# Kernel tuning notes

Hardware: AMD Instinct MI355X
Metric: run time of the kernel (lower is better)

## Reference

```python
import jax, jax.numpy as jnp
import numpy as np
from jax import lax

# dims from init_kwargs: in_features=1920, out_features=1920, window_size=12
B = 1024
IN_F = 1920
OUT_F = 1920
WS = 12              # window_size (GRU input & hidden size)
K = IN_F // WS
OUT_WS = OUT_F // K  # per-block decoder output = 12
D_HID = 1024         # decoder hidden width


def sinusoidal_pe(L, d):
    # standard sinusoidal positional encoding, shape (L, d)
    pos = jnp.arange(L, dtype=jnp.float32)[:, None]
    div = jnp.exp(jnp.arange(0, d, 2, dtype=jnp.float32) * (-np.log(10000.0) / d))
    ang = pos * div  # (L, d//2)
    pe = jnp.zeros((L, d), jnp.float32)
    pe = pe.at[:, 0::2].set(jnp.sin(ang))
    pe = pe.at[:, 1::2].set(jnp.cos(ang))
    return pe


def gru(x, h0, Wih, Whh, bih, bhh):
    # x: (B, T, I) batch_first; PyTorch GRU gate order: r, z, n
    def step(h, xt):
        gi = xt @ Wih.T + bih          # (B, 3H)
        gh = h @ Whh.T + bhh           # (B, 3H)
        ir, iz, inn = jnp.split(gi, 3, axis=-1)
        hr, hz, hn = jnp.split(gh, 3, axis=-1)
        r = jax.nn.sigmoid(ir + hr)
        z = jax.nn.sigmoid(iz + hz)
        n = jnp.tanh(inn + r * hn)
        h_new = (1.0 - z) * n + z * h
        return h_new, h_new
    hT, ys = lax.scan(step, h0, jnp.swapaxes(x, 0, 1))
    return jnp.swapaxes(ys, 0, 1), hT


def setup_inputs() -> dict:
    key = jax.random.key(0)
    ks = jax.random.split(key, 11)
    s = lambda k, shape: jax.random.normal(k, shape, jnp.float32) * 0.05
    return {
        "x": jax.random.normal(ks[0], (B, IN_F), jnp.float32),
        # per-block segment encoders: Linear(WS, WS) x K
        "enc_W": s(ks[1], (K, WS, WS)),
        "enc_b": s(ks[2], (K, WS)),
        # shared GRU (input=hidden=WS)
        "Wih": s(ks[3], (3 * WS, WS)),
        "Whh": s(ks[4], (3 * WS, WS)),
        "bih": s(ks[5], (3 * WS,)),
        "bhh": s(ks[6], (3 * WS,)),
        # per-block decoders: Linear(WS,1024) -> Linear(1024,OUT_WS)
        "dec_W1": s(ks[7], (K, WS, D_HID)),
        "dec_b1": s(ks[8], (K, D_HID)),
        "dec_W2": s(ks[9], (K, D_HID, OUT_WS)),
        "dec_b2": s(ks[10], (K, OUT_WS)),
    }


def reference(x, enc_W, enc_b, Wih, Whh, bih, bhh, dec_W1, dec_b1, dec_W2, dec_b2):
    # SegmentationBlock: split (B, IN_F) -> (B, K, WS), per-block Linear+ReLU
    xb = x.reshape(B, K, WS)
    xs = jax.nn.relu(jnp.einsum('bki,kio->bko', xb, enc_W) + enc_b[None])

    # first GRU pass: only final hidden state h (B, WS)
    h0 = jnp.zeros((B, WS), x.dtype)
    _, h = gru(xs, h0, Wih, Whh, bih, bhh)

    # positional encodings (value-independent sinusoidal, broadcast over batch)
    pos_enc = sinusoidal_pe(K, WS)          # (K, WS)
    ch_pe = sinusoidal_pe(K, K)             # (K, K)
    # channel_enc[:, :, j] = channel_encs[:, :, j // K]  (fused gather)
    channel_enc = ch_pe[:, jnp.arange(WS) // K]  # (K, WS)

    x_enc = xs + pos_enc[None] + channel_enc[None]

    # second GRU pass initialized with h
    out, _ = gru(x_enc, h, Wih, Whh, bih, bhh)  # (B, K, WS)

    # per-block decoder MLPs (dropout is identity in eval)
    hid = jnp.einsum('bkd,kdh->bkh', out, dec_W1) + dec_b1[None]      # (B, K, 1024)
    res = jnp.einsum('bkh,kho->bko', hid, dec_W2) + dec_b2[None]      # (B, K, OUT_WS)
    return res.reshape(B, K * OUT_WS)[:, :OUT_F]
```

## Files before the change

kernel.cpp:

```cpp
#include <hip/hip_runtime.h>
#include <hip/hip_bf16.h>

using bf16 = __hip_bfloat16;
typedef float v2f __attribute__((ext_vector_type(2)));

#define C1 1.44269504f
#define C2 2.88539008f

__device__ __forceinline__ float fexp2(float x) { return __builtin_amdgcn_exp2f(x); }
__device__ __forceinline__ float frcp(float x)  { return __builtin_amdgcn_rcpf(x); }

__device__ __forceinline__ unsigned int f2bfbits(float f) {
    union { float f; unsigned int u; } c; c.f = f;
    return (c.u + 0x7fffu + ((c.u >> 16) & 1u)) >> 16;
}

#define KSTR 12288
#define OFF_PEGI 15728640

__global__ __launch_bounds__(256) void k_encode(
    const float* __restrict__ x, const float* __restrict__ encW, const float* __restrict__ encb,
    const float* __restrict__ Wih, const float* __restrict__ bih, const float* __restrict__ bhh,
    uint2* __restrict__ gi, float4* __restrict__ pegi)
{
    const int k = blockIdx.y, t = threadIdx.x;
    const int b = blockIdx.x * 256 + t;

    __shared__ float sW[144], sbm[12], sWih[432], sbih[36], spet[12];
    __shared__ uint2 st[256 * 13];
    if (t < 144) sW[t]  = encW[k * 144 + t];
    if (t < 12)  sbm[t] = encb[k * 12 + t];
    for (int i = t; i < 432; i += 256) sWih[i] = Wih[i];
    if (t < 36)  sbih[t] = bih[t] + (t < 24 ? bhh[t] : 0.f);
    if (t < 12) {
        int m = t >> 1;
        float div = __expf((float)(2 * m) * (-0.7675283643313489f));
        float ang = (float)k * div;
        spet[t] = ((t & 1) ? cosf(ang) : sinf(ang)) + sinf((float)k);
    }
    __syncthreads();
    if (t < 12 && blockIdx.x == 0) {
        float sr = 0.f, sz = 0.f, sn = 0.f;
        #pragma unroll
        for (int o = 0; o < 12; o++) {
            sr = fmaf(spet[o], sWih[t * 12 + o], sr);
            sz = fmaf(spet[o], sWih[(12 + t) * 12 + o], sz);
            sn = fmaf(spet[o], sWih[(24 + t) * 12 + o], sn);
        }
        pegi[k * 12 + t] = make_float4(C1 * sr, C1 * sz, C2 * sn, 0.f);
    }

    const float4* xp = reinterpret_cast<const float4*>(x + (size_t)b * 1920 + k * 12);
    float4 a0 = xp[0], a1 = xp[1], a2 = xp[2];
    float xv[12] = {a0.x,a0.y,a0.z,a0.w, a1.x,a1.y,a1.z,a1.w, a2.x,a2.y,a2.z,a2.w};

    float xs[12];
    #pragma unroll
    for (int o = 0; o < 12; o++) {
        float s = sbm[o];
        #pragma unroll
        for (int i = 0; i < 12; i++) s = fmaf(xv[i], sW[i * 12 + o], s);
        xs[o] = fmaxf(s, 0.f);
    }

    #pragma unroll
    for (int j = 0; j < 12; j++) {
        float sr = sbih[j], sz = sbih[12 + j], sn = sbih[24 + j];
        #pragma unroll
        for (int o = 0; o < 12; o++) {
            sr = fmaf(xs[o], sWih[j * 12 + o], sr);
            sz = fmaf(xs[o], sWih[(12 + j) * 12 + o], sz);
            sn = fmaf(xs[o], sWih[(24 + j) * 12 + o], sn);
        }
        st[t * 13 + j] = make_uint2(f2bfbits(C1 * sr) | (f2bfbits(C1 * sz) << 16),
                                    f2bfbits(C2 * sn));
    }
    __syncthreads();
    uint2* gbase = gi + (size_t)k * KSTR + (size_t)blockIdx.x * 3072;
    for (int i = t; i < 3072; i += 256) {
        int bl = i / 12;
        gbase[i] = st[bl * 13 + (i - bl * 12)];
    }
}

__global__ __launch_bounds__(64) void k_recur(
    const float* __restrict__ Whh, const float* __restrict__ bhh,
    const uint2* __restrict__ gi, const float4* __restrict__ pegi,
    float* __restrict__ hout)
{
    const int lane = threadIdx.x;
    const int ju = (lane < 12) ? lane : 11;
    const int b = blockIdx.x;

    v2f wr2[6], wz2[6], wn2[6];
    #pragma unroll
    for (int i = 0; i < 6; i++) {
        wr2[i] = (v2f){C1 * Whh[ju * 12 + 2*i],        C1 * Whh[ju * 12 + 2*i + 1]};
        wz2[i] = (v2f){C1 * Whh[(12 + ju) * 12 + 2*i], C1 * Whh[(12 + ju) * 12 + 2*i + 1]};
        wn2[i] = (v2f){C2 * Whh[(24 + ju) * 12 + 2*i], C2 * Whh[(24 + ju) * 12 + 2*i + 1]};
    }
    const float bn = C2 * bhh[24 + ju];

    const uint2* gp = gi + (size_t)b * 12 + ju;

    v2f hs2[6];
    #pragma unroll
    for (int i = 0; i < 6; i++) hs2[i] = (v2f){0.f, 0.f};
    float hself = 0.f, p = 1.f;

    uint2 buf[8];
    #pragma unroll
    for (int i = 0; i < 8; i++) buf[i] = gp[(size_t)i * KSTR];

    for (int ko = 0; ko < 160; ko += 8) {
        #pragma unroll
        for (int i = 0; i < 8; i++) {
            const int k = ko + i;
            const int kp = (k + 8 > 159) ? 159 : k + 8;
            float gr = __int_as_float((int)(buf[i].x << 16));
            float gz = __int_as_float((int)(buf[i].x & 0xffff0000u));
            float gn = __int_as_float((int)(buf[i].y << 16));
            buf[i] = gp[(size_t)kp * KSTR];
            v2f an = (v2f){bn, 0.f};
            v2f ar = (v2f){gr, 0.f};
            v2f az = (v2f){gz, 0.f};
            #pragma unroll
            for (int d = 0; d < 6; d++) an += wn2[d] * hs2[d];
            #pragma unroll
            for (int d = 0; d < 6; d++) { ar += wr2[d] * hs2[d]; az += wz2[d] * hs2[d]; }
            float hr = ar.x + ar.y;
            float hz = az.x + az.y;
            float hn = an.x + an.y;
            float r = frcp(1.f + fexp2(-hr));
            float w = frcp(1.f + fexp2(hz));
            float t = fmaf(r, hn, gn);
            float e = frcp(1.f + fexp2(t));
            float hj = fmaf(w, fmaf(-2.f, e, p), hself);
            hself = hj; p = 1.f - hj;
            int hv = __float_as_int(hj);
            #pragma unroll
            for (int d = 0; d < 6; d++)
                hs2[d] = (v2f){__int_as_float(__builtin_amdgcn_readlane(hv, 2*d)),
                               __int_as_float(__builtin_amdgcn_readlane(hv, 2*d + 1))};
        }
    }

    const float4* pp = pegi + ju;
    float4 pb[8];
    #pragma unroll
    for (int i = 0; i < 8; i++) {
        buf[i] = gp[(size_t)i * KSTR];
        pb[i]  = pp[i * 12];
    }
    float* ho = hout + (size_t)b * 1920;
    for (int ko = 0; ko < 160; ko += 8) {
        #pragma unroll
        for (int i = 0; i < 8; i++) {
            const int k = ko + i;
            const int kp = (k + 8 > 159) ? 159 : k + 8;
            float gr = __int_as_float((int)(buf[i].x << 16))         + pb[i].x;
            float gz = __int_as_float((int)(buf[i].x & 0xffff0000u)) + pb[i].y;
            float gn = __int_as_float((int)(buf[i].y << 16))         + pb[i].z;
            buf[i] = gp[(size_t)kp * KSTR];
            pb[i]  = pp[kp * 12];
            v2f an = (v2f){bn, 0.f};
            v2f ar = (v2f){gr, 0.f};
            v2f az = (v2f){gz, 0.f};
            #pragma unroll
            for (int d = 0; d < 6; d++) an += wn2[d] * hs2[d];
            #pragma unroll
            for (int d = 0; d < 6; d++) { ar += wr2[d] * hs2[d]; az += wz2[d] * hs2[d]; }
            float hr = ar.x + ar.y;
            float hz = az.x + az.y;
            float hn = an.x + an.y;
            float r = frcp(1.f + fexp2(-hr));
            float w = frcp(1.f + fexp2(hz));
            float t = fmaf(r, hn, gn);
            float e = frcp(1.f + fexp2(t));
            float hj = fmaf(w, fmaf(-2.f, e, p), hself);
            hself = hj; p = 1.f - hj;
            if (lane < 12) ho[k * 12 + lane] = hj;
            int hv = __float_as_int(hj);
            #pragma unroll
            for (int d = 0; d < 6; d++)
                hs2[d] = (v2f){__int_as_float(__builtin_amdgcn_readlane(hv, 2*d)),
                               __int_as_float(__builtin_amdgcn_readlane(hv, 2*d + 1))};
        }
    }
}

__global__ __launch_bounds__(256) void k_foldapply(
    const float* __restrict__ W1, const float* __restrict__ b1,
    const float* __restrict__ W2, const float* __restrict__ b2,
    float* __restrict__ out)
{
    const int k = blockIdx.x, t = threadIdx.x;
    __shared__ float sB[12288];
    __shared__ float sb1[1024];
    __shared__ float sWc[144], sbc[12];
    {
        const float4* w2p = reinterpret_cast<const float4*>(W2 + (size_t)k * 12288);
        float4* sB4 = reinterpret_cast<float4*>(sB);
        for (int i = t; i < 3072; i += 256) sB4[i] = w2p[i];
        const float4* b1p = reinterpret_cast<const float4*>(b1 + (size_t)k * 1024);
        float4* sb14 = reinterpret_cast<float4*>(sb1);
        sb14[t] = b1p[t];
    }
    __syncthreads();
    if (t < 156) {
        const int o = (t < 144) ? (t % 12) : (t - 144);
        float s0 = 0.f, s1 = 0.f, s2 = 0.f, s3 = 0.f;
        if (t < 144) {
            const float4* va4 = reinterpret_cast<const float4*>(W1 + (size_t)k * 12288 + (size_t)(t / 12) * 1024);
            #pragma unroll 4
            for (int q = 0; q < 256; q++) {
                float4 a = va4[q];
                const float* bq = sB + q * 48 + o;
                s0 = fmaf(a.x, bq[0],  s0);
                s1 = fmaf(a.y, bq[12], s1);
                s2 = fmaf(a.z, bq[24], s2);
                s3 = fmaf(a.w, bq[36], s3);
            }
        } else {
            #pragma unroll 4
            for (int hh = 0; hh < 1024; hh += 4) {
                const float* bq = sB + hh * 12 + o;
                s0 = fmaf(sb1[hh],     bq[0],  s0);
                s1 = fmaf(sb1[hh + 1], bq[12], s1);
                s2 = fmaf(sb1[hh + 2], bq[24], s2);
                s3 = fmaf(sb1[hh + 3], bq[36], s3);
            }
        }
        float s = (s0 + s1) + (s2 + s3);
        if (t < 144) sWc[t] = s;
        else         sbc[t - 144] = s + b2[k * 12 + o];
    }
    __syncthreads();

    for (int bb = t; bb < 1024; bb += 256) {
        float* hp = out + (size_t)bb * 1920 + k * 12;
        float4* h4 = reinterpret_cast<float4*>(hp);
        float4 a0 = h4[0], a1 = h4[1], a2 = h4[2];
        float hv[12] = {a0.x,a0.y,a0.z,a0.w, a1.x,a1.y,a1.z,a1.w, a2.x,a2.y,a2.z,a2.w};
        float ov[12];
        #pragma unroll
        for (int o = 0; o < 12; o++) {
            float s = sbc[o];
            #pragma unroll
            for (int d = 0; d < 12; d++) s = fmaf(hv[d], sWc[d * 12 + o], s);
            ov[o] = s;
        }
        h4[0] = make_float4(ov[0], ov[1], ov[2],  ov[3]);
        h4[1] = make_float4(ov[4], ov[5], ov[6],  ov[7]);
        h4[2] = make_float4(ov[8], ov[9], ov[10], ov[11]);
    }
}

extern "C" void kernel_launch(void* const* d_in, const int* in_sizes, int n_in,
                              void* d_out, int out_size, void* d_ws, size_t ws_size,
                              hipStream_t stream)
{
    const float* x    = (const float*)d_in[0];
    const float* encW = (const float*)d_in[1];
    const float* encb = (const float*)d_in[2];
    const float* Wih  = (const float*)d_in[3];
    const float* Whh  = (const float*)d_in[4];
    const float* bih  = (const float*)d_in[5];
    const float* bhh  = (const float*)d_in[6];
    const float* W1   = (const float*)d_in[7];
    const float* b1   = (const float*)d_in[8];
    const float* W2   = (const float*)d_in[9];
    const float* b2   = (const float*)d_in[10];
    float* out = (float*)d_out;

    char* ws = (char*)d_ws;
    uint2*  gi   = (uint2*)(ws);
    float4* pegi = (float4*)(ws + OFF_PEGI);

    k_encode   <<<dim3(4, 160), 256, 0, stream>>>(x, encW, encb, Wih, bih, bhh, gi, pegi);
    k_recur    <<<dim3(1024),   64,  0, stream>>>(Whh, bhh, gi, pegi, out);
    k_foldapply<<<dim3(160),    256, 0, stream>>>(W1, b1, W2, b2, out);
}
```

Baseline: 188.3 us.

## Pack four batch rows per wavefront in GRU recurrence using ds_bpermute broadcast

The recurrence kernel now handles four batch samples per 64-lane wavefront, one per 16-lane group, instead of one sample using only 12 of 64 lanes. Each lane gets the hidden state of its own group through ds_bpermute, which replaces the scalar readlane broadcast, and the grid shrinks from 1024 to 256 blocks. This fills more of each wave and cuts the number of waves, but it puts an LDS-crossbar permute with its latency on the serial per-step dependency chain.

```diff
diff --git a/kernel.cpp b/kernel.cpp
--- a/kernel.cpp
+++ b/kernel.cpp
@@ -89,8 +89,14 @@
     float* __restrict__ hout)
 {
     const int lane = threadIdx.x;
-    const int ju = (lane < 12) ? lane : 11;
-    const int b = blockIdx.x;
+    const int grp  = lane >> 4;
+    const int j    = lane & 15;
+    const int ju   = (j < 12) ? j : 11;
+    const int b    = blockIdx.x * 4 + grp;
+
+    int ba[12];
+    #pragma unroll
+    for (int d = 0; d < 12; d++) ba[d] = ((lane & 48) + d) << 2;
 
     v2f wr2[6], wz2[6], wn2[6];
     #pragma unroll
@@ -101,16 +107,16 @@
     }
     const float bn = C2 * bhh[24 + ju];
 
-    const uint2* gp = gi + (size_t)b * 12 + ju;
-
-    v2f hs2[6];
-    #pragma unroll
-    for (int i = 0; i < 6; i++) hs2[i] = (v2f){0.f, 0.f};
+    const int voff = b * 12 + ju;
+
+    v2f h2[6];
+    #pragma unroll
+    for (int i = 0; i < 6; i++) h2[i] = (v2f){0.f, 0.f};
     float hself = 0.f, p = 1.f;
 
     uint2 buf[8];
     #pragma unroll
-    for (int i = 0; i < 8; i++) buf[i] = gp[(size_t)i * KSTR];
+    for (int i = 0; i < 8; i++) buf[i] = gi[(size_t)i * KSTR + voff];
 
     for (int ko = 0; ko < 160; ko += 8) {
         #pragma unroll
@@ -120,14 +126,14 @@
             float gr = __int_as_float((int)(buf[i].x << 16));
             float gz = __int_as_float((int)(buf[i].x & 0xffff0000u));
             float gn = __int_as_float((int)(buf[i].y << 16));
-            buf[i] = gp[(size_t)kp * KSTR];
+            buf[i] = gi[(size_t)kp * KSTR + voff];
             v2f an = (v2f){bn, 0.f};
             v2f ar = (v2f){gr, 0.f};
             v2f az = (v2f){gz, 0.f};
             #pragma unroll
-            for (int d = 0; d < 6; d++) an += wn2[d] * hs2[d];
-            #pragma unroll
-            for (int d = 0; d < 6; d++) { ar += wr2[d] * hs2[d]; az += wz2[d] * hs2[d]; }
+            for (int d = 0; d < 6; d++) an += wn2[d] * h2[d];
+            #pragma unroll
+            for (int d = 0; d < 6; d++) { ar += wr2[d] * h2[d]; az += wz2[d] * h2[d]; }
             float hr = ar.x + ar.y;
             float hz = az.x + az.y;
             float hn = an.x + an.y;
@@ -140,19 +146,18 @@
             int hv = __float_as_int(hj);
             #pragma unroll
             for (int d = 0; d < 6; d++)
-                hs2[d] = (v2f){__int_as_float(__builtin_amdgcn_readlane(hv, 2*d)),
-                               __int_as_float(__builtin_amdgcn_readlane(hv, 2*d + 1))};
-        }
-    }
-
-    const float4* pp = pegi + ju;
+                h2[d] = (v2f){__int_as_float(__builtin_amdgcn_ds_bpermute(ba[2*d],     hv)),
+                              __int_as_float(__builtin_amdgcn_ds_bpermute(ba[2*d + 1], hv))};
+        }
+    }
+
     float4 pb[8];
     #pragma unroll
     for (int i = 0; i < 8; i++) {
-        buf[i] = gp[(size_t)i * KSTR];
-        pb[i]  = pp[i * 12];
-    }
-    float* ho = hout + (size_t)b * 1920;
+        buf[i] = gi[(size_t)i * KSTR + voff];
+        pb[i]  = pegi[i * 12 + ju];
+    }
+    const int hoff = b * 1920 + j;
     for (int ko = 0; ko < 160; ko += 8) {
         #pragma unroll
         for (int i = 0; i < 8; i++) {
@@ -161,15 +166,15 @@
             float gr = __int_as_float((int)(buf[i].x << 16))         + pb[i].x;
             float gz = __int_as_float((int)(buf[i].x & 0xffff0000u)) + pb[i].y;
             float gn = __int_as_float((int)(buf[i].y << 16))         + pb[i].z;
-            buf[i] = gp[(size_t)kp * KSTR];
-            pb[i]  = pp[kp * 12];
+            buf[i] = gi[(size_t)kp * KSTR + voff];
+            pb[i]  = pegi[kp * 12 + ju];
             v2f an = (v2f){bn, 0.f};
             v2f ar = (v2f){gr, 0.f};
             v2f az = (v2f){gz, 0.f};
             #pragma unroll
-            for (int d = 0; d < 6; d++) an += wn2[d] * hs2[d];
-            #pragma unroll
-            for (int d = 0; d < 6; d++) { ar += wr2[d] * hs2[d]; az += wz2[d] * hs2[d]; }
+            for (int d = 0; d < 6; d++) an += wn2[d] * h2[d];
+            #pragma unroll
+            for (int d = 0; d < 6; d++) { ar += wr2[d] * h2[d]; az += wz2[d] * h2[d]; }
             float hr = ar.x + ar.y;
             float hz = az.x + az.y;
             float hn = an.x + an.y;
@@ -179,12 +184,12 @@
             float e = frcp(1.f + fexp2(t));
             float hj = fmaf(w, fmaf(-2.f, e, p), hself);
             hself = hj; p = 1.f - hj;
-            if (lane < 12) ho[k * 12 + lane] = hj;
+            if (j < 12) hout[hoff + k * 12] = hj;
             int hv = __float_as_int(hj);
             #pragma unroll
             for (int d = 0; d < 6; d++)
-                hs2[d] = (v2f){__int_as_float(__builtin_amdgcn_readlane(hv, 2*d)),
-                               __int_as_float(__builtin_amdgcn_readlane(hv, 2*d + 1))};
+                h2[d] = (v2f){__int_as_float(__builtin_amdgcn_ds_bpermute(ba[2*d],     hv)),
+                              __int_as_float(__builtin_amdgcn_ds_bpermute(ba[2*d + 1], hv))};
         }
     }
 }
@@ -278,6 +283,6 @@
     float4* pegi = (float4*)(ws + OFF_PEGI);
 
     k_encode   <<<dim3(4, 160), 256, 0, stream>>>(x, encW, encb, Wih, bih, bhh, gi, pegi);
-    k_recur    <<<dim3(1024),   64,  0, stream>>>(Whh, bhh, gi, pegi, out);
+    k_recur    <<<dim3(256),    64,  0, stream>>>(Whh, bhh, gi, pegi, out);
     k_foldapply<<<dim3(160),    256, 0, stream>>>(W1, b1, W2, b2, out);
 }
```

New measurement: 198.0 us. +5.1%, slower.

## Run GRU recurrence on MFMA with 16 batch rows per wave and fused decoder

Applied to the files above, without the earlier changes.

The GRU hidden-state matvec is rewritten as fp16 16x16x16 MFMA ops, so each 64-lane wave advances 16 batch rows at once instead of one row per wave with readlane broadcasts. The encoder now writes gate inputs in an MFMA-friendly bf16 layout, and the folded decoder weights are packed to fp16 and applied inside the recurrence, which removes the separate read-modify-write pass over the output. The grid shrinks from 1024 waves to 64, which cuts total work but leaves far fewer waves to hide the serial step latency. fp16 weights and hidden state lower precision.

```diff
diff --git a/kernel.cpp b/kernel.cpp
--- a/kernel.cpp
+++ b/kernel.cpp
@@ -2,32 +2,40 @@
 #include <hip/hip_bf16.h>
 
 using bf16 = __hip_bfloat16;
-typedef float v2f __attribute__((ext_vector_type(2)));
+typedef __fp16 half2_t __attribute__((ext_vector_type(2)));
+typedef __fp16 half4_t __attribute__((ext_vector_type(4)));
+typedef float  f4_t    __attribute__((ext_vector_type(4)));
 
 #define C1 1.44269504f
 #define C2 2.88539008f
 
 __device__ __forceinline__ float fexp2(float x) { return __builtin_amdgcn_exp2f(x); }
 __device__ __forceinline__ float frcp(float x)  { return __builtin_amdgcn_rcpf(x); }
-
 __device__ __forceinline__ unsigned int f2bfbits(float f) {
     union { float f; unsigned int u; } c; c.f = f;
     return (c.u + 0x7fffu + ((c.u >> 16) & 1u)) >> 16;
 }
-
-#define KSTR 12288
-#define OFF_PEGI 15728640
+__device__ __forceinline__ unsigned int pk2(float a, float b) {
+    return f2bfbits(a) | (f2bfbits(b) << 16);
+}
+__device__ __forceinline__ float blo(unsigned int u) { return __int_as_float((int)(u << 16)); }
+__device__ __forceinline__ float bhi(unsigned int u) { return __int_as_float((int)(u & 0xffff0000u)); }
+
+#define OFF_GIN  10485760
+#define OFF_PERZ 15728640
+#define OFF_PEN  15892480
+#define OFF_WCA  15974400
 
 __global__ __launch_bounds__(256) void k_encode(
     const float* __restrict__ x, const float* __restrict__ encW, const float* __restrict__ encb,
     const float* __restrict__ Wih, const float* __restrict__ bih, const float* __restrict__ bhh,
-    uint2* __restrict__ gi, float4* __restrict__ pegi)
+    uint4* __restrict__ giRZ, uint2* __restrict__ giN,
+    uint4* __restrict__ peRZ, uint2* __restrict__ peN)
 {
     const int k = blockIdx.y, t = threadIdx.x;
     const int b = blockIdx.x * 256 + t;
 
-    __shared__ float sW[144], sbm[12], sWih[432], sbih[36], spet[12];
-    __shared__ uint2 st[256 * 13];
+    __shared__ float sW[144], sbm[12], sWih[432], sbih[36], spet[12], spe3[36];
     if (t < 144) sW[t]  = encW[k * 144 + t];
     if (t < 12)  sbm[t] = encb[k * 12 + t];
     for (int i = t; i < 432; i += 256) sWih[i] = Wih[i];
@@ -39,7 +47,7 @@
         spet[t] = ((t & 1) ? cosf(ang) : sinf(ang)) + sinf((float)k);
     }
     __syncthreads();
-    if (t < 12 && blockIdx.x == 0) {
+    if (t < 12) {
         float sr = 0.f, sz = 0.f, sn = 0.f;
         #pragma unroll
         for (int o = 0; o < 12; o++) {
@@ -47,7 +55,7 @@
             sz = fmaf(spet[o], sWih[(12 + t) * 12 + o], sz);
             sn = fmaf(spet[o], sWih[(24 + t) * 12 + o], sn);
         }
-        pegi[k * 12 + t] = make_float4(C1 * sr, C1 * sz, C2 * sn, 0.f);
+        spe3[t] = C1 * sr; spe3[12 + t] = C1 * sz; spe3[24 + t] = C2 * sn;
     }
 
     const float4* xp = reinterpret_cast<const float4*>(x + (size_t)b * 1920 + k * 12);
@@ -63,6 +71,7 @@
         xs[o] = fmaxf(s, 0.f);
     }
 
+    float r12[12], z12[12], n12[12];
     #pragma unroll
     for (int j = 0; j < 12; j++) {
         float sr = sbih[j], sz = sbih[12 + j], sn = sbih[24 + j];
@@ -72,127 +81,178 @@
             sz = fmaf(xs[o], sWih[(12 + j) * 12 + o], sz);
             sn = fmaf(xs[o], sWih[(24 + j) * 12 + o], sn);
         }
-        st[t * 13 + j] = make_uint2(f2bfbits(C1 * sr) | (f2bfbits(C1 * sz) << 16),
-                                    f2bfbits(C2 * sn));
+        r12[j] = C1 * sr; z12[j] = C1 * sz; n12[j] = C2 * sn;
     }
     __syncthreads();
-    uint2* gbase = gi + (size_t)k * KSTR + (size_t)blockIdx.x * 3072;
-    for (int i = t; i < 3072; i += 256) {
-        int bl = i / 12;
-        gbase[i] = st[bl * 13 + (i - bl * 12)];
+
+    if (blockIdx.x == 0 && t < 64) {
+        const int q = t >> 4;
+        float vr[4], vz[4], vn[4];
+        #pragma unroll
+        for (int i = 0; i < 4; i++) {
+            int row = 4 * q + i;
+            vr[i] = (row < 12) ? spe3[row]      : 0.f;
+            vz[i] = (row < 12) ? spe3[12 + row] : 0.f;
+            vn[i] = (row < 12) ? spe3[24 + row] : 0.f;
+        }
+        peRZ[k * 64 + t] = make_uint4(pk2(vr[0],vr[1]), pk2(vr[2],vr[3]),
+                                      pk2(vz[0],vz[1]), pk2(vz[2],vz[3]));
+        peN [k * 64 + t] = make_uint2(pk2(vn[0],vn[1]), pk2(vn[2],vn[3]));
+    }
+
+    const int c = b & 15, w = b >> 4;
+    const int base = (k * 64 + w) * 64 + c;
+    #pragma unroll
+    for (int g = 0; g < 3; g++) {
+        giRZ[base + 16 * g] = make_uint4(pk2(r12[4*g], r12[4*g+1]), pk2(r12[4*g+2], r12[4*g+3]),
+                                         pk2(z12[4*g], z12[4*g+1]), pk2(z12[4*g+2], z12[4*g+3]));
+        giN [base + 16 * g] = make_uint2(pk2(n12[4*g], n12[4*g+1]), pk2(n12[4*g+2], n12[4*g+3]));
     }
 }
 
 __global__ __launch_bounds__(64) void k_recur(
     const float* __restrict__ Whh, const float* __restrict__ bhh,
-    const uint2* __restrict__ gi, const float4* __restrict__ pegi,
-    float* __restrict__ hout)
+    const uint4* __restrict__ giRZ, const uint2* __restrict__ giN,
+    const uint4* __restrict__ peRZ, const uint2* __restrict__ peN,
+    const uint2* __restrict__ Wca, float* __restrict__ out)
 {
     const int lane = threadIdx.x;
-    const int ju = (lane < 12) ? lane : 11;
-    const int b = blockIdx.x;
-
-    v2f wr2[6], wz2[6], wn2[6];
-    #pragma unroll
-    for (int i = 0; i < 6; i++) {
-        wr2[i] = (v2f){C1 * Whh[ju * 12 + 2*i],        C1 * Whh[ju * 12 + 2*i + 1]};
-        wz2[i] = (v2f){C1 * Whh[(12 + ju) * 12 + 2*i], C1 * Whh[(12 + ju) * 12 + 2*i + 1]};
-        wn2[i] = (v2f){C2 * Whh[(24 + ju) * 12 + 2*i], C2 * Whh[(24 + ju) * 12 + 2*i + 1]};
-    }
-    const float bn = C2 * bhh[24 + ju];
-
-    const uint2* gp = gi + (size_t)b * 12 + ju;
-
-    v2f hs2[6];
-    #pragma unroll
-    for (int i = 0; i < 6; i++) hs2[i] = (v2f){0.f, 0.f};
-    float hself = 0.f, p = 1.f;
-
-    uint2 buf[8];
-    #pragma unroll
-    for (int i = 0; i < 8; i++) buf[i] = gp[(size_t)i * KSTR];
-
-    for (int ko = 0; ko < 160; ko += 8) {
-        #pragma unroll
-        for (int i = 0; i < 8; i++) {
+    const int c = lane & 15, q = lane >> 4;
+    const int wv = blockIdx.x;
+
+    union HU { half4_t h; half2_t p[2]; uint2 u; };
+    half4_t Ar, Az, An;
+    {
+        float vr[4], vz[4], vn[4];
+        #pragma unroll
+        for (int i = 0; i < 4; i++) {
+            int kd = 4 * q + i;
+            float fr = 0.f, fz = 0.f, fn = 0.f;
+            if (c < 12) {
+                if (kd < 12) {
+                    fr = C1 * Whh[c * 12 + kd];
+                    fz = C1 * Whh[(12 + c) * 12 + kd];
+                    fn = C2 * Whh[(24 + c) * 12 + kd];
+                } else if (kd == 12) {
+                    fn = C2 * bhh[24 + c];
+                }
+            }
+            vr[i] = fr; vz[i] = fz; vn[i] = fn;
+        }
+        HU ur, uz, un;
+        ur.p[0] = __builtin_amdgcn_cvt_pkrtz(vr[0], vr[1]);
+        ur.p[1] = __builtin_amdgcn_cvt_pkrtz(vr[2], vr[3]);
+        uz.p[0] = __builtin_amdgcn_cvt_pkrtz(vz[0], vz[1]);
+        uz.p[1] = __builtin_amdgcn_cvt_pkrtz(vz[2], vz[3]);
+        un.p[0] = __builtin_amdgcn_cvt_pkrtz(vn[0], vn[1]);
+        un.p[1] = __builtin_amdgcn_cvt_pkrtz(vn[2], vn[3]);
+        Ar = ur.h; Az = uz.h; An = un.h;
+    }
+
+    HU B;
+    B.u.x = (q < 3) ? 0u : 0x3C00u;
+    B.u.y = 0u;
+
+    float hsf[4] = {0.f, 0.f, 0.f, 0.f};
+    float pp [4] = {1.f, 1.f, 1.f, 1.f};
+    const f4_t zero4 = {0.f, 0.f, 0.f, 0.f};
+
+    uint4 gRZ[4]; uint2 gN[4];
+    #pragma unroll
+    for (int i = 0; i < 4; i++) {
+        gRZ[i] = giRZ[(i * 64 + wv) * 64 + lane];
+        gN [i] = giN [(i * 64 + wv) * 64 + lane];
+    }
+
+    for (int ko = 0; ko < 160; ko += 4) {
+        #pragma unroll
+        for (int i = 0; i < 4; i++) {
             const int k = ko + i;
-            const int kp = (k + 8 > 159) ? 159 : k + 8;
-            float gr = __int_as_float((int)(buf[i].x << 16));
-            float gz = __int_as_float((int)(buf[i].x & 0xffff0000u));
-            float gn = __int_as_float((int)(buf[i].y << 16));
-            buf[i] = gp[(size_t)kp * KSTR];
-            v2f an = (v2f){bn, 0.f};
-            v2f ar = (v2f){gr, 0.f};
-            v2f az = (v2f){gz, 0.f};
+            const int kp = (k + 4 > 159) ? 159 : k + 4;
+            f4_t Cr = {blo(gRZ[i].x), bhi(gRZ[i].x), blo(gRZ[i].y), bhi(gRZ[i].y)};
+            f4_t Cz = {blo(gRZ[i].z), bhi(gRZ[i].z), blo(gRZ[i].w), bhi(gRZ[i].w)};
+            float Gn[4] = {blo(gN[i].x), bhi(gN[i].x), blo(gN[i].y), bhi(gN[i].y)};
+            gRZ[i] = giRZ[(kp * 64 + wv) * 64 + lane];
+            gN [i] = giN [(kp * 64 + wv) * 64 + lane];
+            f4_t Dr = __builtin_amdgcn_mfma_f32_16x16x16f16(Ar, B.h, Cr, 0, 0, 0);
+            f4_t Dz = __builtin_amdgcn_mfma_f32_16x16x16f16(Az, B.h, Cz, 0, 0, 0);
+            f4_t Dn = __builtin_amdgcn_mfma_f32_16x16x16f16(An, B.h, zero4, 0, 0, 0);
             #pragma unroll
-            for (int d = 0; d < 6; d++) an += wn2[d] * hs2[d];
+            for (int ii = 0; ii < 4; ii++) {
+                float r  = frcp(1.f + fexp2(-Dr[ii]));
+                float w  = frcp(1.f + fexp2(Dz[ii]));
+                float tt = fmaf(r, Dn[ii], Gn[ii]);
+                float e  = frcp(1.f + fexp2(tt));
+                float s  = fmaf(-2.f, e, pp[ii]);
+                float hj = fmaf(w, s, hsf[ii]);
+                hsf[ii] = hj; pp[ii] = 1.f - hj;
+            }
+            HU nb;
+            nb.p[0] = __builtin_amdgcn_cvt_pkrtz(hsf[0], hsf[1]);
+            nb.p[1] = __builtin_amdgcn_cvt_pkrtz(hsf[2], hsf[3]);
+            B.u.x = (q < 3) ? nb.u.x : 0x3C00u;
+            B.u.y = (q < 3) ? nb.u.y : 0u;
+        }
+    }
+
+    uint4 pRZ[4]; uint2 pN[4]; uint2 wc[4];
+    #pragma unroll
+    for (int i = 0; i < 4; i++) {
+        gRZ[i] = giRZ[(i * 64 + wv) * 64 + lane];
+        gN [i] = giN [(i * 64 + wv) * 64 + lane];
+        pRZ[i] = peRZ[i * 64 + lane];
+        pN [i] = peN [i * 64 + lane];
+        wc [i] = Wca [i * 64 + lane];
+    }
+    float* orow = out + ((size_t)wv * 16 + c) * 1920 + 4 * q;
+    for (int ko = 0; ko < 160; ko += 4) {
+        #pragma unroll
+        for (int i = 0; i < 4; i++) {
+            const int k = ko + i;
+            const int kp = (k + 4 > 159) ? 159 : k + 4;
+            f4_t Cr = {blo(gRZ[i].x) + blo(pRZ[i].x), bhi(gRZ[i].x) + bhi(pRZ[i].x),
+                       blo(gRZ[i].y) + blo(pRZ[i].y), bhi(gRZ[i].y) + bhi(pRZ[i].y)};
+            f4_t Cz = {blo(gRZ[i].z) + blo(pRZ[i].z), bhi(gRZ[i].z) + bhi(pRZ[i].z),
+                       blo(gRZ[i].w) + blo(pRZ[i].w), bhi(gRZ[i].w) + bhi(pRZ[i].w)};
+            float Gn[4] = {blo(gN[i].x) + blo(pN[i].x), bhi(gN[i].x) + bhi(pN[i].x),
+                           blo(gN[i].y) + blo(pN[i].y), bhi(gN[i].y) + bhi(pN[i].y)};
+            HU adec; adec.u = wc[i];
+            gRZ[i] = giRZ[(kp * 64 + wv) * 64 + lane];
+            gN [i] = giN [(kp * 64 + wv) * 64 + lane];
+            pRZ[i] = peRZ[kp * 64 + lane];
+            pN [i] = peN [kp * 64 + lane];
+            wc [i] = Wca [kp * 64 + lane];
+            f4_t Dr = __builtin_amdgcn_mfma_f32_16x16x16f16(Ar, B.h, Cr, 0, 0, 0);
+            f4_t Dz = __builtin_amdgcn_mfma_f32_16x16x16f16(Az, B.h, Cz, 0, 0, 0);
+            f4_t Dn = __builtin_amdgcn_mfma_f32_16x16x16f16(An, B.h, zero4, 0, 0, 0);
             #pragma unroll
-            for (int d = 0; d < 6; d++) { ar += wr2[d] * hs2[d]; az += wz2[d] * hs2[d]; }
-            float hr = ar.x + ar.y;
-            float hz = az.x + az.y;
-            float hn = an.x + an.y;
-            float r = frcp(1.f + fexp2(-hr));
-            float w = frcp(1.f + fexp2(hz));
-            float t = fmaf(r, hn, gn);
-            float e = frcp(1.f + fexp2(t));
-            float hj = fmaf(w, fmaf(-2.f, e, p), hself);
-            hself = hj; p = 1.f - hj;
-            int hv = __float_as_int(hj);
-            #pragma unroll
-            for (int d = 0; d < 6; d++)
-                hs2[d] = (v2f){__int_as_float(__builtin_amdgcn_readlane(hv, 2*d)),
-                               __int_as_float(__builtin_amdgcn_readlane(hv, 2*d + 1))};
-        }
-    }
-
-    const float4* pp = pegi + ju;
-    float4 pb[8];
-    #pragma unroll
-    for (int i = 0; i < 8; i++) {
-        buf[i] = gp[(size_t)i * KSTR];
-        pb[i]  = pp[i * 12];
-    }
-    float* ho = hout + (size_t)b * 1920;
-    for (int ko = 0; ko < 160; ko += 8) {
-        #pragma unroll
-        for (int i = 0; i < 8; i++) {
-            const int k = ko + i;
-            const int kp = (k + 8 > 159) ? 159 : k + 8;
-            float gr = __int_as_float((int)(buf[i].x << 16))         + pb[i].x;
-            float gz = __int_as_float((int)(buf[i].x & 0xffff0000u)) + pb[i].y;
-            float gn = __int_as_float((int)(buf[i].y << 16))         + pb[i].z;
-            buf[i] = gp[(size_t)kp * KSTR];
-            pb[i]  = pp[kp * 12];
-            v2f an = (v2f){bn, 0.f};
-            v2f ar = (v2f){gr, 0.f};
-            v2f az = (v2f){gz, 0.f};
-            #pragma unroll
-            for (int d = 0; d < 6; d++) an += wn2[d] * hs2[d];
-            #pragma unroll
-            for (int d = 0; d < 6; d++) { ar += wr2[d] * hs2[d]; az += wz2[d] * hs2[d]; }
-            float hr = ar.x + ar.y;
-            float hz = az.x + az.y;
-            float hn = an.x + an.y;
-            float r = frcp(1.f + fexp2(-hr));
-            float w = frcp(1.f + fexp2(hz));
-            float t = fmaf(r, hn, gn);
-            float e = frcp(1.f + fexp2(t));
-            float hj = fmaf(w, fmaf(-2.f, e, p), hself);
-            hself = hj; p = 1.f - hj;
-            if (lane < 12) ho[k * 12 + lane] = hj;
-            int hv = __float_as_int(hj);
-            #pragma unroll
-            for (int d = 0; d < 6; d++)
-                hs2[d] = (v2f){__int_as_float(__builtin_amdgcn_readlane(hv, 2*d)),
-                               __int_as_float(__builtin_amdgcn_readlane(hv, 2*d + 1))};
-        }
-    }
-}
-
-__global__ __launch_bounds__(256) void k_foldapply(
+            for (int ii = 0; ii < 4; ii++) {
+                float r  = frcp(1.f + fexp2(-Dr[ii]));
+                float w  = frcp(1.f + fexp2(Dz[ii]));
+                float tt = fmaf(r, Dn[ii], Gn[ii]);
+                float e  = frcp(1.f + fexp2(tt));
+                float s  = fmaf(-2.f, e, pp[ii]);
+                float hj = fmaf(w, s, hsf[ii]);
+                hsf[ii] = hj; pp[ii] = 1.f - hj;
+            }
+            HU nb;
+            nb.p[0] = __builtin_amdgcn_cvt_pkrtz(hsf[0], hsf[1]);
+            nb.p[1] = __builtin_amdgcn_cvt_pkrtz(hsf[2], hsf[3]);
+            B.u.x = (q < 3) ? nb.u.x : 0x3C00u;
+            B.u.y = (q < 3) ? nb.u.y : 0u;
+            f4_t O = __builtin_amdgcn_mfma_f32_16x16x16f16(adec.h, B.h, zero4, 0, 0, 0);
+            if (q < 3) {
+                float4* op = reinterpret_cast<float4*>(orow + k * 12);
+                *op = make_float4(O[0], O[1], O[2], O[3]);
+            }
+        }
+    }
+}
+
+__global__ __launch_bounds__(256) void k_fold(
     const float* __restrict__ W1, const float* __restrict__ b1,
     const float* __restrict__ W2, const float* __restrict__ b2,
-    float* __restrict__ out)
+    uint2* __restrict__ Wca)
 {
     const int k = blockIdx.x, t = threadIdx.x;
     __shared__ float sB[12288];
@@ -213,9 +273,9 @@
         if (t < 144) {
             const float4* va4 = reinterpret_cast<const float4*>(W1 + (size_t)k * 12288 + (size_t)(t / 12) * 1024);
             #pragma unroll 4
-            for (int q = 0; q < 256; q++) {
-                float4 a = va4[q];
-                const float* bq = sB + q * 48 + o;
+            for (int qq = 0; qq < 256; qq++) {
+                float4 a = va4[qq];
+                const float* bq = sB + qq * 48 + o;
                 s0 = fmaf(a.x, bq[0],  s0);
                 s1 = fmaf(a.y, bq[12], s1);
                 s2 = fmaf(a.z, bq[24], s2);
@@ -236,23 +296,23 @@
         else         sbc[t - 144] = s + b2[k * 12 + o];
     }
     __syncthreads();
-
-    for (int bb = t; bb < 1024; bb += 256) {
-        float* hp = out + (size_t)bb * 1920 + k * 12;
-        float4* h4 = reinterpret_cast<float4*>(hp);
-        float4 a0 = h4[0], a1 = h4[1], a2 = h4[2];
-        float hv[12] = {a0.x,a0.y,a0.z,a0.w, a1.x,a1.y,a1.z,a1.w, a2.x,a2.y,a2.z,a2.w};
-        float ov[12];
-        #pragma unroll
-        for (int o = 0; o < 12; o++) {
-            float s = sbc[o];
-            #pragma unroll
-            for (int d = 0; d < 12; d++) s = fmaf(hv[d], sWc[d * 12 + o], s);
-            ov[o] = s;
-        }
-        h4[0] = make_float4(ov[0], ov[1], ov[2],  ov[3]);
-        h4[1] = make_float4(ov[4], ov[5], ov[6],  ov[7]);
-        h4[2] = make_float4(ov[8], ov[9], ov[10], ov[11]);
+    if (t < 64) {
+        const int o = t & 15, q = t >> 4;
+        float v[4];
+        #pragma unroll
+        for (int i = 0; i < 4; i++) {
+            int kd = 4 * q + i;
+            float f = 0.f;
+            if (o < 12) {
+                if (kd < 12)       f = sWc[kd * 12 + o];
+                else if (kd == 12) f = sbc[o];
+            }
+            v[i] = f;
+        }
+        union { half2_t p[2]; uint2 u; } pk;
+        pk.p[0] = __builtin_amdgcn_cvt_pkrtz(v[0], v[1]);
+        pk.p[1] = __builtin_amdgcn_cvt_pkrtz(v[2], v[3]);
+        Wca[k * 64 + t] = pk.u;
     }
 }
 
@@ -274,10 +334,13 @@
     float* out = (float*)d_out;
 
     char* ws = (char*)d_ws;
-    uint2*  gi   = (uint2*)(ws);
-    float4* pegi = (float4*)(ws + OFF_PEGI);
-
-    k_encode   <<<dim3(4, 160), 256, 0, stream>>>(x, encW, encb, Wih, bih, bhh, gi, pegi);
-    k_recur    <<<dim3(1024),   64,  0, stream>>>(Whh, bhh, gi, pegi, out);
-    k_foldapply<<<dim3(160),    256, 0, stream>>>(W1, b1, W2, b2, out);
-}
+    uint4* giRZ = (uint4*)(ws);
+    uint2* giN  = (uint2*)(ws + OFF_GIN);
+    uint4* peRZ = (uint4*)(ws + OFF_PERZ);
+    uint2* peN  = (uint2*)(ws + OFF_PEN);
+    uint2* Wca  = (uint2*)(ws + OFF_WCA);
+
+    k_encode<<<dim3(4, 160), 256, 0, stream>>>(x, encW, encb, Wih, bih, bhh, giRZ, giN, peRZ, peN);
+    k_fold  <<<dim3(160),    256, 0, stream>>>(W1, b1, W2, b2, Wca);
+    k_recur <<<dim3(64),     64,  0, stream>>>(Whh, bhh, giRZ, giN, peRZ, peN, Wca, out);
+}
```

Result: slower. 309.1 us (+64.1%).
